# Kernel tuning notes

Measured on AMD Instinct MI355X. Metric: run time of the kernel, lower is better.

Reference implementation:

```python
import jax, jax.numpy as jnp
from jax import lax
import numpy as np

N_X, N_U, N_Y, HID = 8, 2, 2, 64
T, B = 2048, 1024
SCALE = 0.02  # small weights keep the 2048-step recurrence stable


def setup_inputs() -> dict:
    key = jax.random.key(0)
    ks = jax.random.split(key, 12)
    rn = lambda k, shp: SCALE * jax.random.normal(k, shp, dtype=jnp.float32)
    return {
        "u": jax.random.normal(ks[0], (T, B, N_U), dtype=jnp.float32),
        "y": jax.random.normal(ks[1], (T, B, N_Y), dtype=jnp.float32),
        # f_xu MLP: [x;u] -> 64 -> tanh -> n_x
        "Wf1": rn(ks[2], (N_X + N_U, HID)), "bf1": jnp.zeros((HID,), jnp.float32),
        "Wf2": rn(ks[3], (HID, N_X)),       "bf2": jnp.zeros((N_X,), jnp.float32),
        # g_x: linear n_x -> n_y
        "Wg": rn(ks[4], (N_X, N_Y)),        "bg": jnp.zeros((N_Y,), jnp.float32),
        # gain net: n_x -> 64 -> tanh -> n_x*n_y
        "Wk1": rn(ks[5], (N_X, HID)),       "bk1": jnp.zeros((HID,), jnp.float32),
        "Wk2": rn(ks[6], (HID, N_X * N_Y)), "bk2": jnp.zeros((N_X * N_Y,), jnp.float32),
    }


def reference(u, y, Wf1, bf1, Wf2, bf2, Wg, bg, Wk1, bk1, Wk2, bk2):
    b = u.shape[1]

    def step(x, uy):  # x: [B, n_x]
        u_t, y_t = uy
        y_hat = x @ Wg + bg                                   # [B, n_y]
        K = (jnp.tanh(x @ Wk1 + bk1) @ Wk2 + bk2).reshape(b, N_X, N_Y)
        e = y_hat - y_t                                        # [B, n_y]
        dx = jnp.tanh(jnp.concatenate([x, u_t], -1) @ Wf1 + bf1) @ Wf2 + bf2
        x_new = x + dx + jnp.einsum("bxy,by->bx", K, e)
        return x_new, None

    x0 = jnp.zeros((b, N_X), dtype=u.dtype)
    x_last, _ = lax.scan(step, x0, (u, y))
    return x_last
```

## Files before the change

### kernel.cpp

```cpp
#include <hip/hip_runtime.h>


#define T_STEPS 2048
#define B_SZ    1024
#define NX      8
#define HID     64

typedef float v2f __attribute__((ext_vector_type(2)));

__device__ __forceinline__ v2f pk_fma(v2f a, v2f b, v2f c) {
  v2f d;
  asm("v_pk_fma_f32 %0, %1, %2, %3" : "=v"(d) : "v"(a), "v"(b), "v"(c));
  return d;
}
__device__ __forceinline__ void pk_fma_acc(v2f& acc, v2f a, v2f b) {
  asm("v_pk_fma_f32 %0, %1, %2, %0" : "+v"(acc) : "v"(a), "v"(b));
}
__device__ __forceinline__ v2f pk_fma_s0lo(v2f a, v2f b, v2f c) {
  v2f d;
  asm("v_pk_fma_f32 %0, %1, %2, %3 op_sel:[0,0,0] op_sel_hi:[0,1,1]"
      : "=v"(d) : "v"(a), "v"(b), "v"(c));
  return d;
}
__device__ __forceinline__ v2f pk_fma_s0hi(v2f a, v2f b, v2f c) {
  v2f d;
  asm("v_pk_fma_f32 %0, %1, %2, %3 op_sel:[1,0,0] op_sel_hi:[1,1,1]"
      : "=v"(d) : "v"(a), "v"(b), "v"(c));
  return d;
}
__device__ __forceinline__ void pk_fma_acc_s1lo(v2f& acc, v2f a, v2f b) {
  asm("v_pk_fma_f32 %0, %1, %2, %0 op_sel:[0,0,0] op_sel_hi:[1,0,1]"
      : "+v"(acc) : "v"(a), "v"(b));
}
__device__ __forceinline__ void pk_fma_acc_s1hi(v2f& acc, v2f a, v2f b) {
  asm("v_pk_fma_f32 %0, %1, %2, %0 op_sel:[0,1,0] op_sel_hi:[1,1,1]"
      : "+v"(acc) : "v"(a), "v"(b));
}

__device__ __forceinline__ v2f tanh_pair(float pa, float pb) {
  v2f r;
  r[0] = __builtin_amdgcn_rcpf(__builtin_amdgcn_exp2f(pa) + 1.0f);
  r[1] = __builtin_amdgcn_rcpf(__builtin_amdgcn_exp2f(pb) + 1.0f);
  v2f h;
  h[0] = fmaf(-2.0f, r[0], 1.0f);
  h[1] = fmaf(-2.0f, r[1], 1.0f);
  return h;
}

template <int CTRL, int RMASK>
__device__ __forceinline__ float dpp_add(float acc) {
  int moved = __builtin_amdgcn_update_dpp(0, __float_as_int(acc), CTRL, RMASK, 0xf, true);
  return acc + __int_as_float(moved);
}

__device__ __forceinline__ float half_reduce(float c) {
  c = dpp_add<0x111, 0xf>(c);
  c = dpp_add<0x112, 0xf>(c);
  c = dpp_add<0x114, 0xf>(c);
  c = dpp_add<0x118, 0xf>(c);
  c = dpp_add<0x142, 0xa>(c);
  return c;
}

__device__ __forceinline__ void swap32(float& a, float& b) {
  asm("v_permlane32_swap_b32 %0, %1" : "+v"(a), "+v"(b));
}

__device__ __forceinline__ float rlf(float v, int lane) {
  return __int_as_float(__builtin_amdgcn_readlane(__float_as_int(v), lane));
}

__global__ __launch_bounds__(64, 1) void luen_kernel(
    const float* __restrict__ u, const float* __restrict__ y,
    const float* __restrict__ Wf1, const float* __restrict__ bf1,
    const float* __restrict__ Wf2, const float* __restrict__ bf2,
    const float* __restrict__ Wg, const float* __restrict__ bg,
    const float* __restrict__ Wk1, const float* __restrict__ bk1,
    const float* __restrict__ Wk2, const float* __restrict__ bk2,
    float* __restrict__ out) {
  const int eb = blockIdx.x;
  const int h  = threadIdx.x;

  const float TS = 2.885390081777927f;
  const float INV64 = 1.0f / 64.0f;

  v2f wf1p[5];
#pragma unroll
  for (int p = 0; p < 5; ++p)
    wf1p[p] = v2f{TS * Wf1[(2 * p) * HID + h], TS * Wf1[(2 * p + 1) * HID + h]};
  v2f wk1p[4];
#pragma unroll
  for (int p = 0; p < 4; ++p)
    wk1p[p] = v2f{TS * Wk1[(2 * p) * HID + h], TS * Wk1[(2 * p + 1) * HID + h]};

  v2f wf2p[4], bf2sp[4];
#pragma unroll
  for (int p = 0; p < 4; ++p) {
    wf2p[p]  = v2f{Wf2[h * NX + 2 * p], Wf2[h * NX + 2 * p + 1]};
    bf2sp[p] = v2f{INV64 * bf2[2 * p], INV64 * bf2[2 * p + 1]};
  }
  v2f wk2e[4], wk2o[4], bk2se[4], bk2so[4];
#pragma unroll
  for (int p = 0; p < 4; ++p) {
    const float* r = Wk2 + h * (NX * 2);
    wk2e[p]  = v2f{r[4 * p], r[4 * p + 2]};
    wk2o[p]  = v2f{r[4 * p + 1], r[4 * p + 3]};
    bk2se[p] = v2f{INV64 * bk2[4 * p], INV64 * bk2[4 * p + 2]};
    bk2so[p] = v2f{INV64 * bk2[4 * p + 1], INV64 * bk2[4 * p + 3]};
  }
  v2f wgc0[4], wgc1[4];
#pragma unroll
  for (int p = 0; p < 4; ++p) {
    wgc0[p] = v2f{Wg[4 * p], Wg[4 * p + 2]};
    wgc1[p] = v2f{Wg[4 * p + 1], Wg[4 * p + 3]};
  }
  const v2f a0i = v2f{bg[0], 0.0f};
  const v2f a1i = v2f{bg[1], 0.0f};
  const v2f pfi = v2f{TS * bf1[h], 0.0f};
  const v2f pki = v2f{TS * bk1[h], 0.0f};

  float probe = (h < 32) ? 0.0f : 1.0f;
  float zf = 0.0f;
  swap32(probe, zf);
  const bool dir1 = __builtin_amdgcn_readlane(__float_as_int(probe), 32) != 0;
  const int laneA = dir1 ? 63 : 31;
  const int laneB = dir1 ? 31 : 63;

  const v2f* __restrict__ pu = reinterpret_cast<const v2f*>(u) + eb;
  const v2f* __restrict__ py = reinterpret_cast<const v2f*>(y) + eb;
  const int STR = B_SZ;

  v2f x2[4];
#pragma unroll
  for (int p = 0; p < 4; ++p) x2[p] = v2f{0.0f, 0.0f};

  v2f Au[4], Ay[4], Bu[4], By[4];

#define LOADG(SET_u, SET_y)                          \
  {                                                  \
    SET_u[0] = pu[0 * STR]; SET_u[1] = pu[1 * STR];  \
    SET_u[2] = pu[2 * STR]; SET_u[3] = pu[3 * STR];  \
    SET_y[0] = py[0 * STR]; SET_y[1] = py[1 * STR];  \
    SET_y[2] = py[2 * STR]; SET_y[3] = py[3 * STR];  \
    pu += 4 * STR; py += 4 * STR;                    \
  }

#define STEP(CU_, CY_)                                                        \
  {                                                                           \
    const v2f cu = (CU_);                                                     \
    const v2f cy = (CY_);                                                     \
                                    \
    v2f a0 = pk_fma(x2[0], wgc0[0], a0i);                                     \
    v2f a1 = pk_fma(x2[0], wgc1[0], a1i);                                     \
    pk_fma_acc(a0, x2[1], wgc0[1]); pk_fma_acc(a1, x2[1], wgc1[1]);           \
    pk_fma_acc(a0, x2[2], wgc0[2]); pk_fma_acc(a1, x2[2], wgc1[2]);           \
    pk_fma_acc(a0, x2[3], wgc0[3]); pk_fma_acc(a1, x2[3], wgc1[3]);           \
    v2f ep;                                                                   \
    ep[0] = a0[0] + a0[1] - cy[0];                                            \
    ep[1] = a1[0] + a1[1] - cy[1];                                            \
                   \
    v2f pf = pk_fma(x2[0], wf1p[0], pfi);                                     \
    pk_fma_acc(pf, x2[1], wf1p[1]);                                           \
    pk_fma_acc(pf, x2[2], wf1p[2]);                                           \
    pk_fma_acc(pf, x2[3], wf1p[3]);                                           \
    pk_fma_acc(pf, cu, wf1p[4]);                                              \
    v2f pkv = pk_fma(x2[0], wk1p[0], pki);                                    \
    pk_fma_acc(pkv, x2[1], wk1p[1]);                                          \
    pk_fma_acc(pkv, x2[2], wk1p[2]);                                          \
    pk_fma_acc(pkv, x2[3], wk1p[3]);                                          \
    const v2f hp = tanh_pair(pf[0] + pf[1], pkv[0] + pkv[1]);                 \
           \
    float c0, c1, c2, c3, c4, c5, c6, c7;                                     \
    {                                                                         \
      v2f t0 = pk_fma_s0hi(hp, wk2e[0], bk2se[0]);                            \
      v2f t1 = pk_fma_s0hi(hp, wk2o[0], bk2so[0]);                            \
      v2f cp = pk_fma_s0lo(hp, wf2p[0], bf2sp[0]);                            \
      pk_fma_acc_s1lo(cp, t0, ep);                                            \
      pk_fma_acc_s1hi(cp, t1, ep);                                            \
      c0 = cp[0]; c1 = cp[1];                                                 \
    }                                                                         \
    {                                                                         \
      v2f t0 = pk_fma_s0hi(hp, wk2e[1], bk2se[1]);                            \
      v2f t1 = pk_fma_s0hi(hp, wk2o[1], bk2so[1]);                            \
      v2f cp = pk_fma_s0lo(hp, wf2p[1], bf2sp[1]);                            \
      pk_fma_acc_s1lo(cp, t0, ep);                                            \
      pk_fma_acc_s1hi(cp, t1, ep);                                            \
      c2 = cp[0]; c3 = cp[1];                                                 \
    }                                                                         \
    {                                                                         \
      v2f t0 = pk_fma_s0hi(hp, wk2e[2], bk2se[2]);                            \
      v2f t1 = pk_fma_s0hi(hp, wk2o[2], bk2so[2]);                            \
      v2f cp = pk_fma_s0lo(hp, wf2p[2], bf2sp[2]);                            \
      pk_fma_acc_s1lo(cp, t0, ep);                                            \
      pk_fma_acc_s1hi(cp, t1, ep);                                            \
      c4 = cp[0]; c5 = cp[1];                                                 \
    }                                                                         \
    {                                                                         \
      v2f t0 = pk_fma_s0hi(hp, wk2e[3], bk2se[3]);                            \
      v2f t1 = pk_fma_s0hi(hp, wk2o[3], bk2so[3]);                            \
      v2f cp = pk_fma_s0lo(hp, wf2p[3], bf2sp[3]);                            \
      pk_fma_acc_s1lo(cp, t0, ep);                                            \
      pk_fma_acc_s1hi(cp, t1, ep);                                            \
      c6 = cp[0]; c7 = cp[1];                                                 \
    }                                                                         \
                  \
    swap32(c0, c4); float d0 = c0 + c4;                                       \
    swap32(c1, c5); float d1 = c1 + c5;                                       \
    swap32(c2, c6); float d2 = c2 + c6;                                       \
    swap32(c3, c7); float d3 = c3 + c7;                                       \
    d0 = half_reduce(d0); d1 = half_reduce(d1);                               \
    d2 = half_reduce(d2); d3 = half_reduce(d3);                               \
    x2[0][0] += rlf(d0, laneA);                                               \
    x2[0][1] += rlf(d1, laneA);                                               \
    x2[1][0] += rlf(d2, laneA);                                               \
    x2[1][1] += rlf(d3, laneA);                                               \
    x2[2][0] += rlf(d0, laneB);                                               \
    x2[2][1] += rlf(d1, laneB);                                               \
    x2[3][0] += rlf(d2, laneB);                                               \
    x2[3][1] += rlf(d3, laneB);                                               \
  }

  LOADG(Au, Ay);
  LOADG(Bu, By);

  for (int it = 0; it < 255; ++it) {
    STEP(Au[0], Ay[0]); STEP(Au[1], Ay[1]); STEP(Au[2], Ay[2]); STEP(Au[3], Ay[3]);
    LOADG(Au, Ay);
    STEP(Bu[0], By[0]); STEP(Bu[1], By[1]); STEP(Bu[2], By[2]); STEP(Bu[3], By[3]);
    LOADG(Bu, By);
  }
  STEP(Au[0], Ay[0]); STEP(Au[1], Ay[1]); STEP(Au[2], Ay[2]); STEP(Au[3], Ay[3]);
  STEP(Bu[0], By[0]); STEP(Bu[1], By[1]); STEP(Bu[2], By[2]); STEP(Bu[3], By[3]);
#undef STEP
#undef LOADG

  if (h == 0) {
#pragma unroll
    for (int p = 0; p < 4; ++p) {
      out[eb * NX + 2 * p]     = x2[p][0];
      out[eb * NX + 2 * p + 1] = x2[p][1];
    }
  }
}

extern "C" void kernel_launch(void* const* d_in, const int* in_sizes, int n_in,
                              void* d_out, int out_size, void* d_ws, size_t ws_size,
                              hipStream_t stream) {
  const float* u   = (const float*)d_in[0];
  const float* y   = (const float*)d_in[1];
  const float* Wf1 = (const float*)d_in[2];
  const float* bf1 = (const float*)d_in[3];
  const float* Wf2 = (const float*)d_in[4];
  const float* bf2 = (const float*)d_in[5];
  const float* Wg  = (const float*)d_in[6];
  const float* bg  = (const float*)d_in[7];
  const float* Wk1 = (const float*)d_in[8];
  const float* bk1 = (const float*)d_in[9];
  const float* Wk2 = (const float*)d_in[10];
  const float* bk2 = (const float*)d_in[11];

  luen_kernel<<<dim3(B_SZ), dim3(HID), 0, stream>>>(
      u, y, Wf1, bf1, Wf2, bf2, Wg, bg, Wk1, bk1, Wk2, bk2, (float*)d_out);
}
```

Before: 664.0 us.

## Process two independent batch elements per wavefront to interleave recurrence chains

Each 64-lane block now advances two batch elements at once, interleaving their dependent FMA, tanh and cross-lane reduction chains, so the latency of one sequential recurrence can be hidden by the other. The grid is halved to 512 blocks, and u/y are loaded as float4 covering both elements. This trades fewer wavefronts (lower occupancy across 256 CUs) for more instruction-level parallelism inside each wave, and roughly doubles register use.

```diff
diff --git a/kernel.cpp b/kernel.cpp
--- a/kernel.cpp
+++ b/kernel.cpp
@@ -7,6 +7,7 @@
 #define HID     64
 
 typedef float v2f __attribute__((ext_vector_type(2)));
+typedef float v4f __attribute__((ext_vector_type(4)));
 
 __device__ __forceinline__ v2f pk_fma(v2f a, v2f b, v2f c) {
   v2f d;
@@ -78,8 +79,8 @@
     const float* __restrict__ Wk1, const float* __restrict__ bk1,
     const float* __restrict__ Wk2, const float* __restrict__ bk2,
     float* __restrict__ out) {
-  const int eb = blockIdx.x;
-  const int h  = threadIdx.x;
+  const int bid = blockIdx.x;
+  const int h   = threadIdx.x;
 
   const float TS = 2.885390081777927f;
   const float INV64 = 1.0f / 64.0f;
@@ -126,119 +127,126 @@
   const int laneA = dir1 ? 63 : 31;
   const int laneB = dir1 ? 31 : 63;
 
-  const v2f* __restrict__ pu = reinterpret_cast<const v2f*>(u) + eb;
-  const v2f* __restrict__ py = reinterpret_cast<const v2f*>(y) + eb;
-  const int STR = B_SZ;
-
-  v2f x2[4];
-#pragma unroll
-  for (int p = 0; p < 4; ++p) x2[p] = v2f{0.0f, 0.0f};
-
-  v2f Au[4], Ay[4], Bu[4], By[4];
-
-#define LOADG(SET_u, SET_y)                          \
+  const v4f* __restrict__ pu = reinterpret_cast<const v4f*>(u) + bid;
+  const v4f* __restrict__ py = reinterpret_cast<const v4f*>(y) + bid;
+  const int STR4 = B_SZ / 2;
+
+  v2f xA[4], xB[4];
+#pragma unroll
+  for (int p = 0; p < 4; ++p) { xA[p] = v2f{0.0f, 0.0f}; xB[p] = v2f{0.0f, 0.0f}; }
+
+  v4f Gu[4], Gy[4], Hu[4], Hy[4];
+
+#define LOADG(SU_, SY_)                              \
   {                                                  \
-    SET_u[0] = pu[0 * STR]; SET_u[1] = pu[1 * STR];  \
-    SET_u[2] = pu[2 * STR]; SET_u[3] = pu[3 * STR];  \
-    SET_y[0] = py[0 * STR]; SET_y[1] = py[1 * STR];  \
-    SET_y[2] = py[2 * STR]; SET_y[3] = py[3 * STR];  \
-    pu += 4 * STR; py += 4 * STR;                    \
-  }
-
-#define STEP(CU_, CY_)                                                        \
+    SU_[0] = pu[0 * STR4]; SU_[1] = pu[1 * STR4];    \
+    SU_[2] = pu[2 * STR4]; SU_[3] = pu[3 * STR4];    \
+    SY_[0] = py[0 * STR4]; SY_[1] = py[1 * STR4];    \
+    SY_[2] = py[2 * STR4]; SY_[3] = py[3 * STR4];    \
+    pu += 4 * STR4; py += 4 * STR4;                  \
+  }
+
+#define CQ(HP_, EP_, P_, CLO_, CHI_)                                          \
   {                                                                           \
-    const v2f cu = (CU_);                                                     \
-    const v2f cy = (CY_);                                                     \
-                                    \
-    v2f a0 = pk_fma(x2[0], wgc0[0], a0i);                                     \
-    v2f a1 = pk_fma(x2[0], wgc1[0], a1i);                                     \
-    pk_fma_acc(a0, x2[1], wgc0[1]); pk_fma_acc(a1, x2[1], wgc1[1]);           \
-    pk_fma_acc(a0, x2[2], wgc0[2]); pk_fma_acc(a1, x2[2], wgc1[2]);           \
-    pk_fma_acc(a0, x2[3], wgc0[3]); pk_fma_acc(a1, x2[3], wgc1[3]);           \
-    v2f ep;                                                                   \
-    ep[0] = a0[0] + a0[1] - cy[0];                                            \
-    ep[1] = a1[0] + a1[1] - cy[1];                                            \
-                   \
-    v2f pf = pk_fma(x2[0], wf1p[0], pfi);                                     \
-    pk_fma_acc(pf, x2[1], wf1p[1]);                                           \
-    pk_fma_acc(pf, x2[2], wf1p[2]);                                           \
-    pk_fma_acc(pf, x2[3], wf1p[3]);                                           \
-    pk_fma_acc(pf, cu, wf1p[4]);                                              \
-    v2f pkv = pk_fma(x2[0], wk1p[0], pki);                                    \
-    pk_fma_acc(pkv, x2[1], wk1p[1]);                                          \
-    pk_fma_acc(pkv, x2[2], wk1p[2]);                                          \
-    pk_fma_acc(pkv, x2[3], wk1p[3]);                                          \
-    const v2f hp = tanh_pair(pf[0] + pf[1], pkv[0] + pkv[1]);                 \
-           \
-    float c0, c1, c2, c3, c4, c5, c6, c7;                                     \
-    {                                                                         \
-      v2f t0 = pk_fma_s0hi(hp, wk2e[0], bk2se[0]);                            \
-      v2f t1 = pk_fma_s0hi(hp, wk2o[0], bk2so[0]);                            \
-      v2f cp = pk_fma_s0lo(hp, wf2p[0], bf2sp[0]);                            \
-      pk_fma_acc_s1lo(cp, t0, ep);                                            \
-      pk_fma_acc_s1hi(cp, t1, ep);                                            \
-      c0 = cp[0]; c1 = cp[1];                                                 \
-    }                                                                         \
-    {                                                                         \
-      v2f t0 = pk_fma_s0hi(hp, wk2e[1], bk2se[1]);                            \
-      v2f t1 = pk_fma_s0hi(hp, wk2o[1], bk2so[1]);                            \
-      v2f cp = pk_fma_s0lo(hp, wf2p[1], bf2sp[1]);                            \
-      pk_fma_acc_s1lo(cp, t0, ep);                                            \
-      pk_fma_acc_s1hi(cp, t1, ep);                                            \
-      c2 = cp[0]; c3 = cp[1];                                                 \
-    }                                                                         \
-    {                                                                         \
-      v2f t0 = pk_fma_s0hi(hp, wk2e[2], bk2se[2]);                            \
-      v2f t1 = pk_fma_s0hi(hp, wk2o[2], bk2so[2]);                            \
-      v2f cp = pk_fma_s0lo(hp, wf2p[2], bf2sp[2]);                            \
-      pk_fma_acc_s1lo(cp, t0, ep);                                            \
-      pk_fma_acc_s1hi(cp, t1, ep);                                            \
-      c4 = cp[0]; c5 = cp[1];                                                 \
-    }                                                                         \
-    {                                                                         \
-      v2f t0 = pk_fma_s0hi(hp, wk2e[3], bk2se[3]);                            \
-      v2f t1 = pk_fma_s0hi(hp, wk2o[3], bk2so[3]);                            \
-      v2f cp = pk_fma_s0lo(hp, wf2p[3], bf2sp[3]);                            \
-      pk_fma_acc_s1lo(cp, t0, ep);                                            \
-      pk_fma_acc_s1hi(cp, t1, ep);                                            \
-      c6 = cp[0]; c7 = cp[1];                                                 \
-    }                                                                         \
-                  \
-    swap32(c0, c4); float d0 = c0 + c4;                                       \
-    swap32(c1, c5); float d1 = c1 + c5;                                       \
-    swap32(c2, c6); float d2 = c2 + c6;                                       \
-    swap32(c3, c7); float d3 = c3 + c7;                                       \
-    d0 = half_reduce(d0); d1 = half_reduce(d1);                               \
-    d2 = half_reduce(d2); d3 = half_reduce(d3);                               \
-    x2[0][0] += rlf(d0, laneA);                                               \
-    x2[0][1] += rlf(d1, laneA);                                               \
-    x2[1][0] += rlf(d2, laneA);                                               \
-    x2[1][1] += rlf(d3, laneA);                                               \
-    x2[2][0] += rlf(d0, laneB);                                               \
-    x2[2][1] += rlf(d1, laneB);                                               \
-    x2[3][0] += rlf(d2, laneB);                                               \
-    x2[3][1] += rlf(d3, laneB);                                               \
-  }
-
-  LOADG(Au, Ay);
-  LOADG(Bu, By);
+    v2f t0 = pk_fma_s0hi(HP_, wk2e[P_], bk2se[P_]);                           \
+    v2f t1 = pk_fma_s0hi(HP_, wk2o[P_], bk2so[P_]);                           \
+    v2f cp = pk_fma_s0lo(HP_, wf2p[P_], bf2sp[P_]);                           \
+    pk_fma_acc_s1lo(cp, t0, EP_);                                             \
+    pk_fma_acc_s1hi(cp, t1, EP_);                                             \
+    CLO_ = cp[0]; CHI_ = cp[1];                                               \
+  }
+
+#define STEP2(U4_, Y4_)                                                       \
+  {                                                                           \
+    const v4f u4 = (U4_);                                                     \
+    const v4f y4 = (Y4_);                                                     \
+    const v2f cuA = v2f{u4.x, u4.y}, cuB = v2f{u4.z, u4.w};                   \
+    const v2f cyA = v2f{y4.x, y4.y}, cyB = v2f{y4.z, y4.w};                   \
+                                \
+    v2f a0A = pk_fma(xA[0], wgc0[0], a0i);                                    \
+    v2f a0B = pk_fma(xB[0], wgc0[0], a0i);                                    \
+    v2f a1A = pk_fma(xA[0], wgc1[0], a1i);                                    \
+    v2f a1B = pk_fma(xB[0], wgc1[0], a1i);                                    \
+    pk_fma_acc(a0A, xA[1], wgc0[1]); pk_fma_acc(a0B, xB[1], wgc0[1]);         \
+    pk_fma_acc(a1A, xA[1], wgc1[1]); pk_fma_acc(a1B, xB[1], wgc1[1]);         \
+    pk_fma_acc(a0A, xA[2], wgc0[2]); pk_fma_acc(a0B, xB[2], wgc0[2]);         \
+    pk_fma_acc(a1A, xA[2], wgc1[2]); pk_fma_acc(a1B, xB[2], wgc1[2]);         \
+    pk_fma_acc(a0A, xA[3], wgc0[3]); pk_fma_acc(a0B, xB[3], wgc0[3]);         \
+    pk_fma_acc(a1A, xA[3], wgc1[3]); pk_fma_acc(a1B, xB[3], wgc1[3]);         \
+    v2f epA, epB;                                                             \
+    epA[0] = a0A[0] + a0A[1] - cyA[0]; epA[1] = a1A[0] + a1A[1] - cyA[1];     \
+    epB[0] = a0B[0] + a0B[1] - cyB[0]; epB[1] = a1B[0] + a1B[1] - cyB[1];     \
+                              \
+    v2f pfA = pk_fma(xA[0], wf1p[0], pfi);                                    \
+    v2f pfB = pk_fma(xB[0], wf1p[0], pfi);                                    \
+    pk_fma_acc(pfA, xA[1], wf1p[1]); pk_fma_acc(pfB, xB[1], wf1p[1]);         \
+    pk_fma_acc(pfA, xA[2], wf1p[2]); pk_fma_acc(pfB, xB[2], wf1p[2]);         \
+    pk_fma_acc(pfA, xA[3], wf1p[3]); pk_fma_acc(pfB, xB[3], wf1p[3]);         \
+    pk_fma_acc(pfA, cuA, wf1p[4]);   pk_fma_acc(pfB, cuB, wf1p[4]);           \
+    v2f pkA = pk_fma(xA[0], wk1p[0], pki);                                    \
+    v2f pkB = pk_fma(xB[0], wk1p[0], pki);                                    \
+    pk_fma_acc(pkA, xA[1], wk1p[1]); pk_fma_acc(pkB, xB[1], wk1p[1]);         \
+    pk_fma_acc(pkA, xA[2], wk1p[2]); pk_fma_acc(pkB, xB[2], wk1p[2]);         \
+    pk_fma_acc(pkA, xA[3], wk1p[3]); pk_fma_acc(pkB, xB[3], wk1p[3]);         \
+    const v2f hpA = tanh_pair(pfA[0] + pfA[1], pkA[0] + pkA[1]);              \
+    const v2f hpB = tanh_pair(pfB[0] + pfB[1], pkB[0] + pkB[1]);              \
+                                                  \
+    float cA0, cA1, cA2, cA3, cA4, cA5, cA6, cA7;                             \
+    float cB0, cB1, cB2, cB3, cB4, cB5, cB6, cB7;                             \
+    CQ(hpA, epA, 0, cA0, cA1) CQ(hpB, epB, 0, cB0, cB1)                       \
+    CQ(hpA, epA, 1, cA2, cA3) CQ(hpB, epB, 1, cB2, cB3)                       \
+    CQ(hpA, epA, 2, cA4, cA5) CQ(hpB, epB, 2, cB4, cB5)                       \
+    CQ(hpA, epA, 3, cA6, cA7) CQ(hpB, epB, 3, cB6, cB7)                       \
+                    \
+    swap32(cA0, cA4); swap32(cB0, cB4);                                       \
+    swap32(cA1, cA5); swap32(cB1, cB5);                                       \
+    swap32(cA2, cA6); swap32(cB2, cB6);                                       \
+    swap32(cA3, cA7); swap32(cB3, cB7);                                       \
+    float dA0 = cA0 + cA4, dB0 = cB0 + cB4;                                   \
+    float dA1 = cA1 + cA5, dB1 = cB1 + cB5;                                   \
+    float dA2 = cA2 + cA6, dB2 = cB2 + cB6;                                   \
+    float dA3 = cA3 + cA7, dB3 = cB3 + cB7;                                   \
+    dA0 = half_reduce(dA0); dB0 = half_reduce(dB0);                           \
+    dA1 = half_reduce(dA1); dB1 = half_reduce(dB1);                           \
+    dA2 = half_reduce(dA2); dB2 = half_reduce(dB2);                           \
+    dA3 = half_reduce(dA3); dB3 = half_reduce(dB3);                           \
+    xA[0][0] += rlf(dA0, laneA); xB[0][0] += rlf(dB0, laneA);                 \
+    xA[0][1] += rlf(dA1, laneA); xB[0][1] += rlf(dB1, laneA);                 \
+    xA[1][0] += rlf(dA2, laneA); xB[1][0] += rlf(dB2, laneA);                 \
+    xA[1][1] += rlf(dA3, laneA); xB[1][1] += rlf(dB3, laneA);                 \
+    xA[2][0] += rlf(dA0, laneB); xB[2][0] += rlf(dB0, laneB);                 \
+    xA[2][1] += rlf(dA1, laneB); xB[2][1] += rlf(dB1, laneB);                 \
+    xA[3][0] += rlf(dA2, laneB); xB[3][0] += rlf(dB2, laneB);                 \
+    xA[3][1] += rlf(dA3, laneB); xB[3][1] += rlf(dB3, laneB);                 \
+  }
+
+  LOADG(Gu, Gy);
+  LOADG(Hu, Hy);
 
   for (int it = 0; it < 255; ++it) {
-    STEP(Au[0], Ay[0]); STEP(Au[1], Ay[1]); STEP(Au[2], Ay[2]); STEP(Au[3], Ay[3]);
-    LOADG(Au, Ay);
-    STEP(Bu[0], By[0]); STEP(Bu[1], By[1]); STEP(Bu[2], By[2]); STEP(Bu[3], By[3]);
-    LOADG(Bu, By);
-  }
-  STEP(Au[0], Ay[0]); STEP(Au[1], Ay[1]); STEP(Au[2], Ay[2]); STEP(Au[3], Ay[3]);
-  STEP(Bu[0], By[0]); STEP(Bu[1], By[1]); STEP(Bu[2], By[2]); STEP(Bu[3], By[3]);
-#undef STEP
+    STEP2(Gu[0], Gy[0]); STEP2(Gu[1], Gy[1]);
+    STEP2(Gu[2], Gy[2]); STEP2(Gu[3], Gy[3]);
+    LOADG(Gu, Gy);
+    STEP2(Hu[0], Hy[0]); STEP2(Hu[1], Hy[1]);
+    STEP2(Hu[2], Hy[2]); STEP2(Hu[3], Hy[3]);
+    LOADG(Hu, Hy);
+  }
+  STEP2(Gu[0], Gy[0]); STEP2(Gu[1], Gy[1]);
+  STEP2(Gu[2], Gy[2]); STEP2(Gu[3], Gy[3]);
+  STEP2(Hu[0], Hy[0]); STEP2(Hu[1], Hy[1]);
+  STEP2(Hu[2], Hy[2]); STEP2(Hu[3], Hy[3]);
+#undef STEP2
+#undef CQ
 #undef LOADG
 
   if (h == 0) {
+    const int ebA = 2 * bid, ebB = 2 * bid + 1;
 #pragma unroll
     for (int p = 0; p < 4; ++p) {
-      out[eb * NX + 2 * p]     = x2[p][0];
-      out[eb * NX + 2 * p + 1] = x2[p][1];
+      out[ebA * NX + 2 * p]     = xA[p][0];
+      out[ebA * NX + 2 * p + 1] = xA[p][1];
+      out[ebB * NX + 2 * p]     = xB[p][0];
+      out[ebB * NX + 2 * p + 1] = xB[p][1];
     }
   }
 }
@@ -259,6 +267,6 @@
   const float* Wk2 = (const float*)d_in[10];
   const float* bk2 = (const float*)d_in[11];
 
-  luen_kernel<<<dim3(B_SZ), dim3(HID), 0, stream>>>(
+  luen_kernel<<<dim3(B_SZ / 2), dim3(HID), 0, stream>>>(
       u, y, Wf1, bf1, Wf2, bf2, Wg, bg, Wk1, bk1, Wk2, bk2, (float*)d_out);
 }
```

Measured after the change: 1.226 ms. 84.6% more time.
